# Performance work log

Measured on AMD Instinct MI355X. Metric: run time of the kernel, lower is better.

Reference implementation:

```python
import jax, jax.numpy as jnp
import numpy as np

# Static config (matches init_kwargs)
B = 1; Z = 64; H = 64; W = 64; C = 96
NH = 3; WS = 4; SS = 2
N = WS ** 3                      # tokens per 3D window = 64
NW = (Z // WS) * (H // WS) * (W // WS)   # num windows = 4096
SCALE = (C // NH) ** -0.5
EPS = 1e-5


def _rel_pos_index():
    # same construction as WindowAttention3D.__init__ (torch.meshgrid default 'ij')
    coords = np.stack(np.meshgrid(np.arange(WS), np.arange(WS), np.arange(WS), indexing='ij'))
    cf = coords.reshape(3, -1)                       # (3, N)
    rc = (cf[:, :, None] - cf[:, None, :]).transpose(1, 2, 0)  # (N, N, 3)
    rc[:, :, 0] += WS - 1; rc[:, :, 1] += WS - 1; rc[:, :, 2] += WS - 1
    rc[:, :, 0] *= (2 * WS - 1) ** 2
    rc[:, :, 1] *= (2 * WS - 1)
    return rc.sum(-1)                                # (N, N) int


def _attn_mask():
    # shifted-window mask, as in SwinTransformerBlock3D.__init__
    img = np.zeros((Z, H, W), dtype=np.float32)
    sl = (slice(0, -WS), slice(-WS, -SS), slice(-SS, None))
    cnt = 0
    for z in sl:
        for h in sl:
            for w in sl:
                img[z, h, w] = cnt
                cnt += 1
    mw = img.reshape(Z // WS, WS, H // WS, WS, W // WS, WS)
    mw = mw.transpose(0, 2, 4, 1, 3, 5).reshape(-1, N)        # (nW, N)
    am = mw[:, None, :] - mw[:, :, None]                      # (nW, N, N)
    return np.where(am != 0, np.float32(-100.0), np.float32(0.0))


REL_IDX = jnp.asarray(_rel_pos_index())        # (N, N) int32, closed-over constant
ATTN_MASK = jnp.asarray(_attn_mask())          # (nW, N, N) float32


def _layernorm(x, g, b):
    m = x.mean(-1, keepdims=True)
    v = ((x - m) ** 2).mean(-1, keepdims=True)
    return (x - m) * jax.lax.rsqrt(v + EPS) * g + b


def _window_partition(x):
    # (B, Z, H, W, C) -> (B*nW, N, C)
    x = x.reshape(B, Z // WS, WS, H // WS, WS, W // WS, WS, C)
    return x.transpose(0, 1, 3, 5, 2, 4, 6, 7).reshape(-1, N, C)


def _window_reverse(wins):
    # (B*nW, N, C) -> (B, Z, H, W, C)
    x = wins.reshape(B, Z // WS, H // WS, W // WS, WS, WS, WS, C)
    return x.transpose(0, 1, 4, 2, 5, 3, 6, 7).reshape(B, Z, H, W, C)


def setup_inputs() -> dict:
    key = jax.random.key(0)
    ks = jax.random.split(key, 8)
    d = {
        'x': jax.random.normal(ks[0], (B, Z * H * W, C), jnp.float32),
        'norm1_w': jnp.ones((C,), jnp.float32),
        'norm1_b': jnp.zeros((C,), jnp.float32),
        'qkv_w': jax.random.normal(ks[1], (3 * C, C), jnp.float32) * 0.02,
        'qkv_b': jnp.zeros((3 * C,), jnp.float32),
        'rel_bias': jax.random.normal(ks[2], ((2 * WS - 1) ** 3, NH), jnp.float32) * 0.02,
        'proj_w': jax.random.normal(ks[3], (C, C), jnp.float32) * 0.02,
        'proj_b': jnp.zeros((C,), jnp.float32),
        'norm2_w': jnp.ones((C,), jnp.float32),
        'norm2_b': jnp.zeros((C,), jnp.float32),
        'fc1_w': jax.random.normal(ks[4], (4 * C, C), jnp.float32) * 0.02,
        'fc1_b': jnp.zeros((4 * C,), jnp.float32),
        'fc2_w': jax.random.normal(ks[5], (C, 4 * C), jnp.float32) * 0.02,
        'fc2_b': jnp.zeros((C,), jnp.float32),
    }
    return d


def reference(x, norm1_w, norm1_b, qkv_w, qkv_b, rel_bias, proj_w, proj_b,
              norm2_w, norm2_b, fc1_w, fc1_b, fc2_w, fc2_b):
    shortcut = x
    h = _layernorm(x, norm1_w, norm1_b).reshape(B, Z, H, W, C)
    # cyclic shift (SW-MSA)
    h = jnp.roll(h, (-SS, -SS, -SS), axis=(1, 2, 3))
    xw = _window_partition(h)                                  # (B*nW, N, C)
    qkv = (xw @ qkv_w.T + qkv_b).reshape(-1, N, 3, NH, C // NH)
    qkv = qkv.transpose(2, 0, 3, 1, 4)                         # (3, B_, NH, N, hd)
    q, k, v = qkv[0] * SCALE, qkv[1], qkv[2]
    attn = jnp.einsum('bhnd,bhmd->bhnm', q, k)                 # (B_, NH, N, N)
    bias = rel_bias[REL_IDX.reshape(-1)].reshape(N, N, NH).transpose(2, 0, 1)
    attn = attn + bias[None]
    attn = attn.reshape(B, NW, NH, N, N) + ATTN_MASK[None, :, None]
    attn = jax.nn.softmax(attn.reshape(-1, NH, N, N), axis=-1)
    out = jnp.einsum('bhnm,bhmd->bhnd', attn, v)
    out = out.transpose(0, 2, 1, 3).reshape(-1, N, C)
    out = out @ proj_w.T + proj_b
    h = _window_reverse(out)
    h = jnp.roll(h, (SS, SS, SS), axis=(1, 2, 3)).reshape(B, Z * H * W, C)
    x = shortcut + h                                            # residual (drop_path=0)
    y = _layernorm(x, norm2_w, norm2_b)
    y = jax.nn.gelu(y @ fc1_w.T + fc1_b, approximate=False)
    y = y @ fc2_w.T + fc2_b
    return x + y
```

## Files before the change

### kernel.cpp

```cpp
#include <hip/hip_runtime.h>

typedef __attribute__((ext_vector_type(8))) short short8;
typedef __attribute__((ext_vector_type(4))) float f32x4;

static __device__ __forceinline__ unsigned short f2bf(float f) {
  return (unsigned short)((__builtin_bit_cast(unsigned int, f) + 0x8000u) >> 16);
}
static __device__ __forceinline__ float bf2f(unsigned short u) {
  return __builtin_bit_cast(float, ((unsigned)u) << 16);
}
static __device__ __forceinline__ unsigned cvtpk(float a, float b) {
  unsigned r;
  asm("v_cvt_pk_bf16_f32 %0, %1, %2" : "=v"(r) : "v"(a), "v"(b));
  return r;
}

constexpr float LOG2E = 1.4426950408889634f;
constexpr float QSCL = 0.17677669529663687f * LOG2E;
constexpr int XP = 104;
constexpr int KP = 104;
constexpr int VTP = 72;

static __device__ __forceinline__ int frag_src(int o, int K) {
  const int j = o & 7;
  const int lane = (o >> 3) & 63;
  const int f = o >> 9;
  const int nks = K >> 5;
  const int ks = f % nks;
  const int t = f / nks;
  const int row = t * 16 + (lane & 15);
  const int k = ks * 32 + (lane >> 4) * 8 + j;
  return row * K + k;
}

__global__ void prep_kernel(const float* __restrict__ qkvw, const float* __restrict__ projw,
                            const float* __restrict__ fc1w, const float* __restrict__ fc2w,
                            const float* __restrict__ relbias,
                            unsigned short* __restrict__ ws, float* __restrict__ tab) {
  int i = blockIdx.x * 256 + threadIdx.x;
  if (i < 27648) ws[i] = f2bf(qkvw[frag_src(i, 96)]);
  if (i < 9216)  ws[27648 + i] = f2bf(projw[frag_src(i, 96)]);
  if (i < 36864) {
    ws[36864 + i] = f2bf(fc1w[frag_src(i, 96)]);
    ws[73728 + i] = f2bf(fc2w[frag_src(i, 384)]);
  }
  if (i < 98304) {
    const int r = i & 3, kgi = (i >> 2) & 3, q = (i >> 4) & 63, nt = (i >> 10) & 3;
    const int vh = i >> 12;
    const int h = vh % 3, v = vh / 3;
    const int key = nt * 16 + kgi * 4 + r;
    const bool bz = v & 4, bh = v & 2, bw = v & 1;
    const int iz = q >> 4, ih = (q >> 2) & 3, iw = q & 3;
    const int jz = key >> 4, jh = (key >> 2) & 3, jw = key & 3;
    const int idx = (iz - jz + 3) * 49 + (ih - jh + 3) * 7 + (iw - jw + 3);
    const int ci = (bz ? (iz < 2 ? 9 : 18) : 0) + (bh ? (ih < 2 ? 3 : 6) : 0) +
                   (bw ? (iw < 2 ? 1 : 2) : 0);
    const int cj = (bz ? (jz < 2 ? 9 : 18) : 0) + (bh ? (jh < 2 ? 3 : 6) : 0) +
                   (bw ? (jw < 2 ? 1 : 2) : 0);
    tab[i] = (relbias[idx * 3 + h] + (ci != cj ? -100.f : 0.f)) * LOG2E;
  }
}

__global__ __launch_bounds__(256, 4) void fused_kernel(
    const float* __restrict__ x,
    const float* __restrict__ n1w, const float* __restrict__ n1b,
    const float* __restrict__ qkvb, const float* __restrict__ tab,
    const float* __restrict__ projb,
    const float* __restrict__ n2w, const float* __restrict__ n2b,
    const float* __restrict__ b1, const float* __restrict__ b2,
    const unsigned short* __restrict__ wq, const unsigned short* __restrict__ wp,
    const unsigned short* __restrict__ w1, const unsigned short* __restrict__ w2,
    float* __restrict__ out) {
  __shared__ unsigned short Xo[64 * XP];
  __shared__ unsigned short Kb[64 * KP];
  __shared__ unsigned short Vt[96 * VTP];

  const int tid = threadIdx.x;
  const int bid = blockIdx.x;
  const int wz = bid >> 8, wh = (bid >> 4) & 15, ww = bid & 15;
  const int wave = tid >> 6, lane = tid & 63;
  const int ln = lane & 15, kg = lane >> 4;

  {
    const int n = tid >> 2, part = tid & 3;
    const int lz = n >> 4, lh = (n >> 2) & 3, lw = n & 3;
    const int sz = (wz * 4 + lz + 2) & 63;
    const int sh = (wh * 4 + lh + 2) & 63;
    const int sw = (ww * 4 + lw + 2) & 63;
    const float* px = x + (size_t)((sz * 64 + sh) * 64 + sw) * 96 + part * 24;
    float4 v[6];
#pragma unroll
    for (int j = 0; j < 6; ++j) v[j] = ((const float4*)px)[j];
    float s = 0.f, sq = 0.f;
#pragma unroll
    for (int j = 0; j < 6; ++j) {
      s += v[j].x + v[j].y + v[j].z + v[j].w;
      sq += v[j].x * v[j].x + v[j].y * v[j].y + v[j].z * v[j].z + v[j].w * v[j].w;
    }
    s += __shfl_xor(s, 1);  s += __shfl_xor(s, 2);
    sq += __shfl_xor(sq, 1); sq += __shfl_xor(sq, 2);
    const float mean = s * (1.f / 96.f);
    const float var = sq * (1.f / 96.f) - mean * mean;
    const float rs = rsqrtf(var + 1e-5f);
    const float4* g4 = (const float4*)(n1w + part * 24);
    const float4* b4 = (const float4*)(n1b + part * 24);
#pragma unroll
    for (int j = 0; j < 6; ++j) {
      float4 g = g4[j], b = b4[j];
      uint2 o;
      o.x = cvtpk((v[j].x - mean) * rs * g.x + b.x, (v[j].y - mean) * rs * g.y + b.y);
      o.y = cvtpk((v[j].z - mean) * rs * g.z + b.z, (v[j].w - mean) * rs * g.w + b.w);
      *(uint2*)&Xo[n * XP + part * 24 + j * 4] = o;
    }
  }

  short8 qa[3];
  {
    short8 a[3];
#pragma unroll
    for (int ks = 0; ks < 3; ++ks)
      a[ks] = *(const short8*)&Xo[(wave * 16 + ln) * XP + ks * 32 + kg * 8];
#pragma unroll
    for (int g = 0; g < 3; ++g) {
      short8 wf[6];
#pragma unroll
      for (int f = 0; f < 6; ++f)
        wf[f] = *(const short8*)&wq[(size_t)(g * 6 + f) * 512 + lane * 8];
#pragma unroll
      for (int t = 0; t < 2; ++t) {
        const int nt = g * 2 + t;
        const int oc = nt * 16 + ln;
        f32x4 acc = {0.f, 0.f, 0.f, 0.f};
#pragma unroll
        for (int ks = 0; ks < 3; ++ks)
          acc = __builtin_amdgcn_mfma_f32_16x16x32_bf16(a[ks], wf[t * 3 + ks], acc, 0, 0, 0);
        const float bias = qkvb[oc];
#pragma unroll
        for (int r = 0; r < 4; ++r)
          Kb[(wave * 16 + kg * 4 + r) * KP + oc] = f2bf((acc[r] + bias) * QSCL);
      }
    }
#pragma unroll
    for (int h = 0; h < 3; ++h)
      qa[h] = *(const short8*)&Kb[(wave * 16 + ln) * KP + h * 32 + kg * 8];
#pragma unroll
    for (int g = 0; g < 3; ++g) {
      short8 wf[6];
#pragma unroll
      for (int f = 0; f < 6; ++f)
        wf[f] = *(const short8*)&wq[(size_t)(18 + g * 6 + f) * 512 + lane * 8];
#pragma unroll
      for (int t = 0; t < 2; ++t) {
        const int nt = g * 2 + t;
        const int oc = 96 + nt * 16 + ln;
        f32x4 acc = {0.f, 0.f, 0.f, 0.f};
#pragma unroll
        for (int ks = 0; ks < 3; ++ks)
          acc = __builtin_amdgcn_mfma_f32_16x16x32_bf16(a[ks], wf[t * 3 + ks], acc, 0, 0, 0);
        const float bias = qkvb[oc];
#pragma unroll
        for (int r = 0; r < 4; ++r)
          Kb[(wave * 16 + kg * 4 + r) * KP + nt * 16 + ln] = f2bf(acc[r] + bias);
      }
    }
#pragma unroll
    for (int g = 0; g < 3; ++g) {
      short8 wf[6];
#pragma unroll
      for (int f = 0; f < 6; ++f)
        wf[f] = *(const short8*)&wq[(size_t)(36 + g * 6 + f) * 512 + lane * 8];
#pragma unroll
      for (int t = 0; t < 2; ++t) {
        const int nt = g * 2 + t;
        const int oc = 192 + nt * 16 + ln;
        f32x4 acc = {0.f, 0.f, 0.f, 0.f};
#pragma unroll
        for (int ks = 0; ks < 3; ++ks)
          acc = __builtin_amdgcn_mfma_f32_16x16x32_bf16(a[ks], wf[t * 3 + ks], acc, 0, 0, 0);
        const float bias = qkvb[oc];
        uint2 u;
        u.x = cvtpk(acc[0] + bias, acc[1] + bias);
        u.y = cvtpk(acc[2] + bias, acc[3] + bias);
        *(uint2*)&Vt[(nt * 16 + ln) * VTP + wave * 16 + kg * 4] = u;
      }
    }
  }
  __syncthreads();

  const int vv = ((wz == 15) ? 4 : 0) | ((wh == 15) ? 2 : 0) | ((ww == 15) ? 1 : 0);
  const float* tb0 = tab + (size_t)(vv * 3) * 4096;
  const int rowbase = wave * 16 + kg * 4;
  const int lA = ((kg & 1) << 5) + ln;
  const int lB = lA + 16;
#pragma unroll
  for (int h = 0; h < 3; ++h) {
    const float* tb = tb0 + h * 4096;
    f32x4 e[4];
#pragma unroll
    for (int nt = 0; nt < 4; ++nt) {
      short8 kf = *(const short8*)&Kb[(nt * 16 + ln) * KP + h * 32 + kg * 8];
      f32x4 trow = *(const f32x4*)(tb + nt * 1024 + (wave * 16 + ln) * 16 + kg * 4);
      f32x4 z = {0.f, 0.f, 0.f, 0.f};
      f32x4 st = __builtin_amdgcn_mfma_f32_16x16x32_bf16(kf, qa[h], z, 0, 0, 0);
#pragma unroll
      for (int r = 0; r < 4; ++r)
        e[nt][r] = __builtin_amdgcn_exp2f(st[r] + trow[r]);
    }
    float hs = 0.f;
#pragma unroll
    for (int nt = 0; nt < 4; ++nt)
#pragma unroll
      for (int r = 0; r < 4; ++r) hs += e[nt][r];
    hs += __shfl_xor(hs, 16);
    hs += __shfl_xor(hs, 32);
    const float inv = __builtin_amdgcn_rcpf(hs);
    unsigned pp[4][2];
#pragma unroll
    for (int nt = 0; nt < 4; ++nt) {
      pp[nt][0] = cvtpk(e[nt][0] * inv, e[nt][1] * inv);
      pp[nt][1] = cvtpk(e[nt][2] * inv, e[nt][3] * inv);
    }
    short8 paf[2];
#pragma unroll
    for (int ks = 0; ks < 2; ++ks) {
      const unsigned a0 = __shfl((int)pp[2 * ks][0], lA);
      const unsigned a1 = __shfl((int)pp[2 * ks][1], lA);
      const unsigned a2 = __shfl((int)pp[2 * ks][0], lB);
      const unsigned a3 = __shfl((int)pp[2 * ks][1], lB);
      const unsigned b0 = __shfl((int)pp[2 * ks + 1][0], lA);
      const unsigned b1 = __shfl((int)pp[2 * ks + 1][1], lA);
      const unsigned b2 = __shfl((int)pp[2 * ks + 1][0], lB);
      const unsigned b3 = __shfl((int)pp[2 * ks + 1][1], lB);
      const bool hi = (kg >> 1) != 0;
      uint4 wv;
      wv.x = hi ? b0 : a0;
      wv.y = hi ? b1 : a1;
      wv.z = hi ? b2 : a2;
      wv.w = hi ? b3 : a3;
      paf[ks] = __builtin_bit_cast(short8, wv);
    }
#pragma unroll
    for (int dt = 0; dt < 2; ++dt) {
      f32x4 oacc = {0.f, 0.f, 0.f, 0.f};
#pragma unroll
      for (int ks = 0; ks < 2; ++ks) {
        short8 vb = *(const short8*)&Vt[(h * 32 + dt * 16 + ln) * VTP + ks * 32 + kg * 8];
        oacc = __builtin_amdgcn_mfma_f32_16x16x32_bf16(paf[ks], vb, oacc, 0, 0, 0);
      }
#pragma unroll
      for (int r = 0; r < 4; ++r)
        Xo[(rowbase + r) * XP + h * 32 + dt * 16 + ln] = f2bf(oacc[r]);
    }
  }
  __syncthreads();

  unsigned short* X2b = Vt;

  int gtok[4];
  float mean_[4], rs_[4];
  {
#pragma unroll
    for (int r = 0; r < 4; ++r) {
      const int n = rowbase + r;
      const int lz = n >> 4, lh = (n >> 2) & 3, lw = n & 3;
      const int oz = (wz * 4 + lz + 2) & 63;
      const int oh = (wh * 4 + lh + 2) & 63;
      const int ow = (ww * 4 + lw + 2) & 63;
      gtok[r] = (oz * 64 + oh) * 64 + ow;
    }
    short8 oa[3];
#pragma unroll
    for (int ks = 0; ks < 3; ++ks)
      oa[ks] = *(const short8*)&Xo[(wave * 16 + ln) * XP + ks * 32 + kg * 8];
    float s_[4] = {0.f, 0.f, 0.f, 0.f}, sq_[4] = {0.f, 0.f, 0.f, 0.f};
#pragma unroll
    for (int g = 0; g < 3; ++g) {
      short8 wf[6];
#pragma unroll
      for (int f = 0; f < 6; ++f)
        wf[f] = *(const short8*)&wp[(size_t)(g * 6 + f) * 512 + lane * 8];
#pragma unroll
      for (int t = 0; t < 2; ++t) {
        const int nt = g * 2 + t;
        const int col = nt * 16 + ln;
        f32x4 acc = {0.f, 0.f, 0.f, 0.f};
#pragma unroll
        for (int ks = 0; ks < 3; ++ks)
          acc = __builtin_amdgcn_mfma_f32_16x16x32_bf16(oa[ks], wf[t * 3 + ks], acc, 0, 0, 0);
        const float pbv = projb[col];
#pragma unroll
        for (int r = 0; r < 4; ++r) {
          const float v = x[(size_t)gtok[r] * 96 + col] + acc[r] + pbv;
          s_[r] += v;
          sq_[r] += v * v;
          X2b[(rowbase + r) * XP + col] = f2bf(v);
        }
      }
    }
#pragma unroll
    for (int r = 0; r < 4; ++r) {
      float s = s_[r], sq = sq_[r];
      s += __shfl_xor(s, 1);  s += __shfl_xor(s, 2);
      s += __shfl_xor(s, 4);  s += __shfl_xor(s, 8);
      sq += __shfl_xor(sq, 1); sq += __shfl_xor(sq, 2);
      sq += __shfl_xor(sq, 4); sq += __shfl_xor(sq, 8);
      const float mean = s * (1.f / 96.f);
      const float var = sq * (1.f / 96.f) - mean * mean;
      mean_[r] = mean;
      rs_[r] = rsqrtf(var + 1e-5f);
    }
  }
#pragma unroll
  for (int nt = 0; nt < 6; ++nt) {
    const int col = nt * 16 + ln;
    const float gw = n2w[col], gb = n2b[col];
#pragma unroll
    for (int r = 0; r < 4; ++r) {
      const float v = bf2f(X2b[(rowbase + r) * XP + col]);
      const float xl = (v - mean_[r]) * rs_[r] * gw + gb;
      Xo[(rowbase + r) * XP + col] = f2bf(xl);
    }
  }

  short8 a2[3];
#pragma unroll
  for (int ks = 0; ks < 3; ++ks)
    a2[ks] = *(const short8*)&Xo[(wave * 16 + ln) * XP + ks * 32 + kg * 8];

  __syncthreads();

  f32x4 facc[6];
#pragma unroll
  for (int nt = 0; nt < 6; ++nt) facc[nt] = (f32x4){0.f, 0.f, 0.f, 0.f};
#pragma unroll 1
  for (int c = 0; c < 4; ++c) {
#pragma unroll
    for (int nt2 = 0; nt2 < 6; ++nt2) {
      short8 wf1[3];
#pragma unroll
      for (int ks = 0; ks < 3; ++ks)
        wf1[ks] = *(const short8*)&w1[(size_t)(c * 18 + nt2 * 3 + ks) * 512 + lane * 8];
      f32x4 acc = {0.f, 0.f, 0.f, 0.f};
#pragma unroll
      for (int ks = 0; ks < 3; ++ks)
        acc = __builtin_amdgcn_mfma_f32_16x16x32_bf16(a2[ks], wf1[ks], acc, 0, 0, 0);
      const float bb = b1[c * 96 + nt2 * 16 + ln];
#pragma unroll
      for (int r = 0; r < 4; ++r) {
        const float v = acc[r] + bb;
        const float t2 = v * v;
        float p = fmaf(0.004287f, t2, -0.05694f);
        p = fmaf(p, t2, 0.3952f);
        float phi = fmaf(p, v, 0.5f);
        phi = fminf(fmaxf(phi, 0.f), 1.f);
        Kb[(rowbase + r) * KP + nt2 * 16 + ln] = f2bf(v * phi);
      }
    }
#pragma unroll
    for (int ks2 = 0; ks2 < 3; ++ks2) {
      short8 pa = *(const short8*)&Kb[(wave * 16 + ln) * KP + ks2 * 32 + kg * 8];
#pragma unroll
      for (int g2 = 0; g2 < 2; ++g2) {
        short8 wf2[3];
#pragma unroll
        for (int t = 0; t < 3; ++t)
          wf2[t] = *(const short8*)&w2[(size_t)((g2 * 3 + t) * 12 + c * 3 + ks2) * 512 + lane * 8];
#pragma unroll
        for (int t = 0; t < 3; ++t)
          facc[g2 * 3 + t] =
              __builtin_amdgcn_mfma_f32_16x16x32_bf16(pa, wf2[t], facc[g2 * 3 + t], 0, 0, 0);
      }
    }
  }
#pragma unroll
  for (int nt = 0; nt < 6; ++nt) {
    const int col = nt * 16 + ln;
    const float bb = b2[col];
#pragma unroll
    for (int r = 0; r < 4; ++r) {
      const float v = bf2f(X2b[(rowbase + r) * XP + col]);
      out[(size_t)gtok[r] * 96 + col] = v + facc[nt][r] + bb;
    }
  }
}

extern "C" void kernel_launch(void* const* d_in, const int* in_sizes, int n_in,
                              void* d_out, int out_size, void* d_ws, size_t ws_size,
                              hipStream_t stream) {
  const float* x    = (const float*)d_in[0];
  const float* n1w  = (const float*)d_in[1];
  const float* n1b  = (const float*)d_in[2];
  const float* qkvw = (const float*)d_in[3];
  const float* qkvb = (const float*)d_in[4];
  const float* relb = (const float*)d_in[5];
  const float* pw   = (const float*)d_in[6];
  const float* pb   = (const float*)d_in[7];
  const float* n2w  = (const float*)d_in[8];
  const float* n2b  = (const float*)d_in[9];
  const float* w1   = (const float*)d_in[10];
  const float* b1   = (const float*)d_in[11];
  const float* w2   = (const float*)d_in[12];
  const float* b2   = (const float*)d_in[13];
  float* out = (float*)d_out;

  unsigned short* wsq = (unsigned short*)d_ws;
  unsigned short* wsp = wsq + 27648;
  unsigned short* ws1 = wsp + 9216;
  unsigned short* ws2 = ws1 + 36864;
  float* tab = (float*)(wsq + 110592);

  hipLaunchKernelGGL(prep_kernel, dim3(384), dim3(256), 0, stream,
                     qkvw, pw, w1, w2, relb, wsq, tab);
  hipLaunchKernelGGL(fused_kernel, dim3(4096), dim3(256), 0, stream,
                     x, n1w, n1b, qkvb, tab, pb, n2w, n2b, b1, b2,
                     wsq, wsp, ws1, ws2, out);
}
```

Measured before the change: 160.1 us.

## Split K/V projection and MLP across waves by output column tiles

The K/V projection and both MLP GEMMs change partitioning. Before, each wave computed its own 16 rows across every output column and loaded every weight fragment. Now each wave owns a subset of output column tiles across all 64 rows, so each weight fragment is fetched by one wave instead of four. The price is extra __syncthreads between phases and inside each MLP chunk, plus reading the A operand for all rows from LDS, and the occupancy hint is lowered from 4 to 3 blocks so each thread can hold more registers.

```diff
diff --git a/kernel.cpp b/kernel.cpp
--- a/kernel.cpp
+++ b/kernel.cpp
@@ -61,7 +61,7 @@
   }
 }
 
-__global__ __launch_bounds__(256, 4) void fused_kernel(
+__global__ __launch_bounds__(256, 3) void fused_kernel(
     const float* __restrict__ x,
     const float* __restrict__ n1w, const float* __restrict__ n1b,
     const float* __restrict__ qkvb, const float* __restrict__ tab,
@@ -143,45 +143,40 @@
 #pragma unroll
     for (int h = 0; h < 3; ++h)
       qa[h] = *(const short8*)&Kb[(wave * 16 + ln) * KP + h * 32 + kg * 8];
-#pragma unroll
-    for (int g = 0; g < 3; ++g) {
-      short8 wf[6];
-#pragma unroll
-      for (int f = 0; f < 6; ++f)
-        wf[f] = *(const short8*)&wq[(size_t)(18 + g * 6 + f) * 512 + lane * 8];
-#pragma unroll
-      for (int t = 0; t < 2; ++t) {
-        const int nt = g * 2 + t;
-        const int oc = 96 + nt * 16 + ln;
+  }
+  __syncthreads();
+
+  {
+    const int t0 = wave < 2 ? 6 + 2 * wave : 8 + wave;
+    const int t1 = wave < 2 ? 7 + 2 * wave : 10 + 2 * wave;
+    const int t2 = wave < 2 ? 12 + wave : 11 + 2 * wave;
+#pragma unroll
+    for (int i = 0; i < 3; ++i) {
+      const int tile = i == 0 ? t0 : (i == 1 ? t1 : t2);
+      const int oc = tile * 16 + ln;
+      short8 wf[3];
+#pragma unroll
+      for (int ks = 0; ks < 3; ++ks)
+        wf[ks] = *(const short8*)&wq[(size_t)(tile * 3 + ks) * 512 + lane * 8];
+      const float bias = qkvb[oc];
+#pragma unroll
+      for (int rt = 0; rt < 4; ++rt) {
         f32x4 acc = {0.f, 0.f, 0.f, 0.f};
 #pragma unroll
-        for (int ks = 0; ks < 3; ++ks)
-          acc = __builtin_amdgcn_mfma_f32_16x16x32_bf16(a[ks], wf[t * 3 + ks], acc, 0, 0, 0);
-        const float bias = qkvb[oc];
-#pragma unroll
-        for (int r = 0; r < 4; ++r)
-          Kb[(wave * 16 + kg * 4 + r) * KP + nt * 16 + ln] = f2bf(acc[r] + bias);
-      }
-    }
-#pragma unroll
-    for (int g = 0; g < 3; ++g) {
-      short8 wf[6];
-#pragma unroll
-      for (int f = 0; f < 6; ++f)
-        wf[f] = *(const short8*)&wq[(size_t)(36 + g * 6 + f) * 512 + lane * 8];
-#pragma unroll
-      for (int t = 0; t < 2; ++t) {
-        const int nt = g * 2 + t;
-        const int oc = 192 + nt * 16 + ln;
-        f32x4 acc = {0.f, 0.f, 0.f, 0.f};
-#pragma unroll
-        for (int ks = 0; ks < 3; ++ks)
-          acc = __builtin_amdgcn_mfma_f32_16x16x32_bf16(a[ks], wf[t * 3 + ks], acc, 0, 0, 0);
-        const float bias = qkvb[oc];
-        uint2 u;
-        u.x = cvtpk(acc[0] + bias, acc[1] + bias);
-        u.y = cvtpk(acc[2] + bias, acc[3] + bias);
-        *(uint2*)&Vt[(nt * 16 + ln) * VTP + wave * 16 + kg * 4] = u;
+        for (int ks = 0; ks < 3; ++ks) {
+          short8 a = *(const short8*)&Xo[(rt * 16 + ln) * XP + ks * 32 + kg * 8];
+          acc = __builtin_amdgcn_mfma_f32_16x16x32_bf16(a, wf[ks], acc, 0, 0, 0);
+        }
+        if (tile < 12) {
+#pragma unroll
+          for (int r = 0; r < 4; ++r)
+            Kb[(rt * 16 + kg * 4 + r) * KP + (tile - 12 + 6) * 16 + ln] = f2bf(acc[r] + bias);
+        } else {
+          uint2 u;
+          u.x = cvtpk(acc[0] + bias, acc[1] + bias);
+          u.y = cvtpk(acc[2] + bias, acc[3] + bias);
+          *(uint2*)&Vt[((tile - 12) * 16 + ln) * VTP + rt * 16 + kg * 4] = u;
+        }
       }
     }
   }
@@ -256,9 +251,8 @@
 
   unsigned short* X2b = Vt;
 
-  int gtok[4];
-  float mean_[4], rs_[4];
   {
+    int gtok[4];
 #pragma unroll
     for (int r = 0; r < 4; ++r) {
       const int n = rowbase + r;
@@ -306,80 +300,104 @@
       sq += __shfl_xor(sq, 4); sq += __shfl_xor(sq, 8);
       const float mean = s * (1.f / 96.f);
       const float var = sq * (1.f / 96.f) - mean * mean;
-      mean_[r] = mean;
-      rs_[r] = rsqrtf(var + 1e-5f);
-    }
-  }
-#pragma unroll
-  for (int nt = 0; nt < 6; ++nt) {
-    const int col = nt * 16 + ln;
-    const float gw = n2w[col], gb = n2b[col];
-#pragma unroll
-    for (int r = 0; r < 4; ++r) {
-      const float v = bf2f(X2b[(rowbase + r) * XP + col]);
-      const float xl = (v - mean_[r]) * rs_[r] * gw + gb;
-      Xo[(rowbase + r) * XP + col] = f2bf(xl);
-    }
-  }
-
-  short8 a2[3];
-#pragma unroll
-  for (int ks = 0; ks < 3; ++ks)
-    a2[ks] = *(const short8*)&Xo[(wave * 16 + ln) * XP + ks * 32 + kg * 8];
-
-  __syncthreads();
-
-  f32x4 facc[6];
-#pragma unroll
-  for (int nt = 0; nt < 6; ++nt) facc[nt] = (f32x4){0.f, 0.f, 0.f, 0.f};
+      const float rs = rsqrtf(var + 1e-5f);
+      s_[r] = mean;
+      sq_[r] = rs;
+    }
+#pragma unroll
+    for (int nt = 0; nt < 6; ++nt) {
+      const int col = nt * 16 + ln;
+      const float gw = n2w[col], gb = n2b[col];
+#pragma unroll
+      for (int r = 0; r < 4; ++r) {
+        const float v = bf2f(X2b[(rowbase + r) * XP + col]);
+        const float xl = (v - s_[r]) * sq_[r] * gw + gb;
+        Xo[(rowbase + r) * XP + col] = f2bf(xl);
+      }
+    }
+  }
+
+  const int nf1 = (wave < 2) ? 1 : 2;
+  const int f1base = (wave < 2) ? wave : 2 + 2 * (wave - 2);
+  const int nf2 = (wave < 2) ? 2 : 1;
+  const int f2base = (wave < 2) ? 2 * wave : 2 + wave;
+  f32x4 acc2[2][4];
+#pragma unroll
+  for (int i = 0; i < 2; ++i)
+#pragma unroll
+    for (int rt = 0; rt < 4; ++rt) acc2[i][rt] = (f32x4){0.f, 0.f, 0.f, 0.f};
+
 #pragma unroll 1
   for (int c = 0; c < 4; ++c) {
-#pragma unroll
-    for (int nt2 = 0; nt2 < 6; ++nt2) {
-      short8 wf1[3];
-#pragma unroll
-      for (int ks = 0; ks < 3; ++ks)
-        wf1[ks] = *(const short8*)&w1[(size_t)(c * 18 + nt2 * 3 + ks) * 512 + lane * 8];
-      f32x4 acc = {0.f, 0.f, 0.f, 0.f};
-#pragma unroll
-      for (int ks = 0; ks < 3; ++ks)
-        acc = __builtin_amdgcn_mfma_f32_16x16x32_bf16(a2[ks], wf1[ks], acc, 0, 0, 0);
-      const float bb = b1[c * 96 + nt2 * 16 + ln];
-#pragma unroll
-      for (int r = 0; r < 4; ++r) {
-        const float v = acc[r] + bb;
-        const float t2 = v * v;
-        float p = fmaf(0.004287f, t2, -0.05694f);
-        p = fmaf(p, t2, 0.3952f);
-        float phi = fmaf(p, v, 0.5f);
-        phi = fminf(fmaxf(phi, 0.f), 1.f);
-        Kb[(rowbase + r) * KP + nt2 * 16 + ln] = f2bf(v * phi);
-      }
-    }
-#pragma unroll
-    for (int ks2 = 0; ks2 < 3; ++ks2) {
-      short8 pa = *(const short8*)&Kb[(wave * 16 + ln) * KP + ks2 * 32 + kg * 8];
-#pragma unroll
-      for (int g2 = 0; g2 < 2; ++g2) {
-        short8 wf2[3];
-#pragma unroll
-        for (int t = 0; t < 3; ++t)
-          wf2[t] = *(const short8*)&w2[(size_t)((g2 * 3 + t) * 12 + c * 3 + ks2) * 512 + lane * 8];
-#pragma unroll
-        for (int t = 0; t < 3; ++t)
-          facc[g2 * 3 + t] =
-              __builtin_amdgcn_mfma_f32_16x16x32_bf16(pa, wf2[t], facc[g2 * 3 + t], 0, 0, 0);
-      }
-    }
-  }
-#pragma unroll
-  for (int nt = 0; nt < 6; ++nt) {
-    const int col = nt * 16 + ln;
-    const float bb = b2[col];
-#pragma unroll
-    for (int r = 0; r < 4; ++r) {
-      const float v = bf2f(X2b[(rowbase + r) * XP + col]);
-      out[(size_t)gtok[r] * 96 + col] = v + facc[nt][r] + bb;
+    __syncthreads();
+#pragma unroll
+    for (int i = 0; i < 2; ++i) {
+      if (i < nf1) {
+        const int tile = f1base + i;
+        short8 wf1[3];
+#pragma unroll
+        for (int ks = 0; ks < 3; ++ks)
+          wf1[ks] = *(const short8*)&w1[(size_t)(c * 18 + tile * 3 + ks) * 512 + lane * 8];
+        const float bb = b1[c * 96 + tile * 16 + ln];
+#pragma unroll
+        for (int rt = 0; rt < 4; ++rt) {
+          f32x4 acc = {0.f, 0.f, 0.f, 0.f};
+#pragma unroll
+          for (int ks = 0; ks < 3; ++ks) {
+            short8 a = *(const short8*)&Xo[(rt * 16 + ln) * XP + ks * 32 + kg * 8];
+            acc = __builtin_amdgcn_mfma_f32_16x16x32_bf16(a, wf1[ks], acc, 0, 0, 0);
+          }
+#pragma unroll
+          for (int r = 0; r < 4; ++r) {
+            const float v = acc[r] + bb;
+            const float t2 = v * v;
+            float p = fmaf(0.004287f, t2, -0.05694f);
+            p = fmaf(p, t2, 0.3952f);
+            float phi = fmaf(p, v, 0.5f);
+            phi = fminf(fmaxf(phi, 0.f), 1.f);
+            Kb[(rt * 16 + kg * 4 + r) * KP + tile * 16 + ln] = f2bf(v * phi);
+          }
+        }
+      }
+    }
+    __syncthreads();
+#pragma unroll
+    for (int ks = 0; ks < 3; ++ks) {
+      short8 wf2[2];
+#pragma unroll
+      for (int i = 0; i < 2; ++i)
+        if (i < nf2)
+          wf2[i] = *(const short8*)&w2[(size_t)((f2base + i) * 12 + c * 3 + ks) * 512 + lane * 8];
+#pragma unroll
+      for (int rt = 0; rt < 4; ++rt) {
+        short8 pa = *(const short8*)&Kb[(rt * 16 + ln) * KP + ks * 32 + kg * 8];
+#pragma unroll
+        for (int i = 0; i < 2; ++i)
+          if (i < nf2)
+            acc2[i][rt] = __builtin_amdgcn_mfma_f32_16x16x32_bf16(pa, wf2[i], acc2[i][rt], 0, 0, 0);
+      }
+    }
+  }
+
+#pragma unroll
+  for (int i = 0; i < 2; ++i) {
+    if (i < nf2) {
+      const int col = (f2base + i) * 16 + ln;
+      const float bb = b2[col];
+#pragma unroll
+      for (int rt = 0; rt < 4; ++rt) {
+#pragma unroll
+        for (int r = 0; r < 4; ++r) {
+          const int n = rt * 16 + kg * 4 + r;
+          const int lz = n >> 4, lh = (n >> 2) & 3, lw = n & 3;
+          const int oz = (wz * 4 + lz + 2) & 63;
+          const int oh = (wh * 4 + lh + 2) & 63;
+          const int ow = (ww * 4 + lw + 2) & 63;
+          const size_t gt = (size_t)((oz * 64 + oh) * 64 + ow);
+          const float v = bf2f(X2b[n * XP + col]);
+          out[gt * 96 + col] = v + acc2[i][rt][r] + bb;
+        }
+      }
     }
   }
 }
```

New measurement: 139.0 us. 13.1% less time.
